# Kernel optimization log

Hardware: AMD Instinct MI355X
Metric: run time of the kernel (lower is better)

## Reference

```python
import jax, jax.numpy as jnp
import numpy as np

# Fixed deterministic sample of 8 offsets from the radius-4 ring (|dx|>1 or |dy|>1, not center).
# The torch module samples these randomly each step; we freeze them for reproducibility.
OFFSETS = [(-4, -4), (-4, -1), (-4, 2), (-3, 4), (-2, -3), (2, 3), (3, -2), (4, 4)]

B, C, H, W = 4, 16, 512, 512
DM, GH = 16, 32  # d_model, gating_hidden


def conv1x1(x, w, b):
    # 1x1 conv == per-pixel matmul: x [B,Cin,H,W], w [Cout,Cin], b [Cout]
    return jnp.einsum('bchw,dc->bdhw', x, w) + b[None, :, None, None]


def setup_inputs() -> dict:
    key = jax.random.key(0)
    ks = jax.random.split(key, 12)
    s_c = 1.0 / np.sqrt(C)
    s_2c = 1.0 / np.sqrt(2 * C)
    s_gh = 1.0 / np.sqrt(GH)
    return {
        'x': jax.random.normal(ks[0], (B, C, H, W), jnp.float32),
        'qw': jax.random.normal(ks[1], (DM, C), jnp.float32) * s_c,
        'qb': jnp.zeros((DM,), jnp.float32),
        'kw': jax.random.normal(ks[2], (DM, C), jnp.float32) * s_c,
        'kb': jnp.zeros((DM,), jnp.float32),
        'mw': jax.random.normal(ks[3], (C, C), jnp.float32) * s_c,
        'mb': jnp.zeros((C,), jnp.float32),
        'scaling': jnp.asarray(np.sqrt(DM), jnp.float32),
        'g1w': jax.random.normal(ks[4], (GH, 2 * C), jnp.float32) * s_2c,
        'g1b': jnp.zeros((GH,), jnp.float32),
        'g2w': jax.random.normal(ks[5], (C, GH), jnp.float32) * s_gh,
        'g2b': jnp.zeros((C,), jnp.float32),
    }


def reference(x, qw, qb, kw, kb, mw, mb, scaling, g1w, g1b, g2w, g2b):
    Q = conv1x1(x, qw, qb)            # [B,DM,H,W]
    K = conv1x1(x, kw, kb)            # [B,DM,H,W]
    M = conv1x1(x, mw, mb)            # [B,C,H,W]
    Q_pooled = Q.mean(axis=(2, 3))    # [B,DM]
    K_pooled = K.mean(axis=(2, 3))    # [B,DM]
    # torch.roll is circular, so the spatial mean of a rolled K equals K_pooled exactly;
    # every offset therefore produces the identical affinity (same math, cheaper).
    attn = (Q_pooled * K_pooled).sum(axis=1) / (scaling + 1e-6)   # [B]
    n = len(OFFSETS)
    # roll-based neighbor gather of messages: [n,B,C,H,W]
    msgs = jnp.stack([jnp.roll(M, (dy, dx), axis=(2, 3)) for dy, dx in OFFSETS], axis=0)
    affinities = jnp.broadcast_to(attn[None, :], (n, attn.shape[0]))  # [n,B]
    w = jax.nn.softmax(affinities, axis=0)[:, :, None, None, None]    # [n,B,1,1,1]
    agg = (msgs * w).sum(axis=0)                                      # [B,C,H,W]
    concat = jnp.concatenate([x, agg], axis=1)                        # [B,2C,H,W]
    hidden = jax.nn.relu(conv1x1(concat, g1w, g1b))                   # [B,GH,H,W]
    gate = jax.nn.sigmoid(conv1x1(hidden, g2w, g2b))                  # [B,C,H,W]
    return agg * gate
```

## Files before the change

kernel.cpp:

```cpp
#include <hip/hip_runtime.h>


#define HW 262144

typedef _Float16 half8  __attribute__((ext_vector_type(8)));
typedef float    f32x4  __attribute__((ext_vector_type(4)));

#define MFMA16(A, B, C) __builtin_amdgcn_mfma_f32_16x16x32_f16((A), (B), (C), 0, 0, 0)

__global__ __launch_bounds__(256, 2) void ga_main(
    const float* __restrict__ x,
    const float* __restrict__ mw,  const float* __restrict__ mb,
    const float* __restrict__ g1w, const float* __restrict__ g1b,
    const float* __restrict__ g2w, const float* __restrict__ g2b,
    float* __restrict__ out)
{
  constexpr int DY[8] = {-4, -4, -4, -3, -2, 2, 3, 4};
  constexpr int DX[8] = {-4, -1,  2,  4, -3, 3, -2, 4};

  __shared__ _Float16 u_s[4 * 64 * 40];
  __shared__ float    w1a[32 * 16];
  __shared__ float    b1s[32];

  const int tid  = threadIdx.x;
  const int wv   = tid >> 6, lane = tid & 63;
  const int q    = lane >> 4, m = lane & 15;

  for (int idx = tid; idx < 512; idx += 256) {
    const int j = idx >> 4, c = idx & 15;
    float s = 0.f;
#pragma unroll
    for (int t2 = 0; t2 < 16; ++t2)
      s += g1w[j * 32 + 16 + t2] * mw[t2 * 16 + c];
    w1a[idx] = s;
  }
  if (tid < 32) {
    float s = g1b[tid];
#pragma unroll
    for (int t2 = 0; t2 < 16; ++t2)
      s += g1w[tid * 32 + 16 + t2] * mb[t2];
    b1s[tid] = s;
  }
  __syncthreads();

  const int j0 = 8 * (m >> 2) + (m & 3);
  const int j1 = j0 + 4;
  half8 aAg_h, aAg_l, aH0_h, aH0_l, aH1_h, aH1_l, aG2_h, aG2_l;
#pragma unroll
  for (int e = 0; e < 8; ++e) {
    const int kk = 8 * q + e;
    float v0 = 0.f;
    if (kk >= 16) v0 = mw[m * 16 + (kk - 16)];
    _Float16 h = (_Float16)v0;
    aAg_h[e] = h; aAg_l[e] = (_Float16)(v0 - (float)h);

    float v1, v2;
    if (kk < 16) { v1 = g1w[j0 * 32 + kk];        v2 = g1w[j1 * 32 + kk]; }
    else         { v1 = w1a[j0 * 16 + (kk - 16)]; v2 = w1a[j1 * 16 + (kk - 16)]; }
    h = (_Float16)v1; aH0_h[e] = h; aH0_l[e] = (_Float16)(v1 - (float)h);
    h = (_Float16)v2; aH1_h[e] = h; aH1_l[e] = (_Float16)(v2 - (float)h);

    const float v3 = g2w[m * 32 + kk];
    h = (_Float16)v3; aG2_h[e] = h; aG2_l[e] = (_Float16)(v3 - (float)h);
  }
  f32x4 bias0, bias1, bias2, bias3;
#pragma unroll
  for (int rg = 0; rg < 4; ++rg) {
    bias0[rg] = mb[4 * q + rg];
    bias1[rg] = b1s[8 * q + rg];
    bias2[rg] = b1s[8 * q + 4 + rg];
    bias3[rg] = g2b[4 * q + rg];
  }

  const int swz = ((blockIdx.x & 7) << 9) | (blockIdx.x >> 3);
  const int b   = swz >> 10;
  const int rem = swz & 1023;
  const int row = rem >> 1;
  const int colbase = ((rem & 1) << 8) + wv * 64;
  const int cw  = colbase + lane;

  const float* xb = x + b * 16 * HW;
  unsigned off[8];
#pragma unroll
  for (int i = 0; i < 8; ++i)
    off[i] = ((row - DY[i]) & 511) * 512 + ((cw - DX[i]) & 511);
  const unsigned ctr = row * 512 + cw;

  float xc[16], xa[16];
#pragma unroll
  for (int c = 0; c < 16; ++c) {
    const float* xp = xb + c * HW;
    xc[c] = xp[ctr];
    float s = 0.f;
#pragma unroll
    for (int i = 0; i < 8; ++i) s += xp[off[i]];
    xa[c] = s * 0.125f;
  }

  _Float16* ub = u_s + (wv * 64 + lane) * 40;
#pragma unroll
  for (int j = 0; j < 4; ++j) {
    half8 v;
#pragma unroll
    for (int e = 0; e < 8; ++e) {
      const int k = j * 8 + e;
      v[e] = (_Float16)((k < 16) ? xc[k] : xa[k - 16]);
    }
    *(half8*)(ub + j * 8) = v;
  }

  const _Float16* ubase = u_s + wv * 64 * 40;
  half8 bf[4];
#pragma unroll
  for (int g = 0; g < 4; ++g)
    bf[g] = *(const half8*)(ubase + (g * 16 + m) * 40 + q * 8);

  float* ob = out + b * 16 * HW + row * 512 + colbase;
  const f32x4 z = {0.f, 0.f, 0.f, 0.f};

#pragma unroll
  for (int g = 0; g < 4; ++g) {
    f32x4 acc_a  = MFMA16(aAg_l, bf[g], z);
    acc_a        = MFMA16(aAg_h, bf[g], acc_a);
    f32x4 acc_h0 = MFMA16(aH0_l, bf[g], z);
    acc_h0       = MFMA16(aH0_h, bf[g], acc_h0);
    f32x4 acc_h1 = MFMA16(aH1_l, bf[g], z);
    acc_h1       = MFMA16(aH1_h, bf[g], acc_h1);

    half8 gB;
#pragma unroll
    for (int rg = 0; rg < 4; ++rg) {
      gB[rg]     = (_Float16)fmaxf(acc_h0[rg] + bias1[rg], 0.f);
      gB[4 + rg] = (_Float16)fmaxf(acc_h1[rg] + bias2[rg], 0.f);
    }

    f32x4 acc_g = MFMA16(aG2_l, gB, z);
    acc_g       = MFMA16(aG2_h, gB, acc_g);

#pragma unroll
    for (int rg = 0; rg < 4; ++rg) {
      const float ag = acc_a[rg] + bias0[rg];
      const float gp = acc_g[rg] + bias3[rg];
      const float gt = __builtin_amdgcn_rcpf(1.f + __expf(-gp));
      ob[(4 * q + rg) * HW + g * 16 + m] = ag * gt;
    }
  }
}

extern "C" void kernel_launch(void* const* d_in, const int* in_sizes, int n_in,
                              void* d_out, int out_size, void* d_ws, size_t ws_size,
                              hipStream_t stream) {
  const float* x   = (const float*)d_in[0];
  const float* mw  = (const float*)d_in[5];
  const float* mb  = (const float*)d_in[6];
  const float* g1w = (const float*)d_in[8];
  const float* g1b = (const float*)d_in[9];
  const float* g2w = (const float*)d_in[10];
  const float* g2b = (const float*)d_in[11];
  float* out = (float*)d_out;

  ga_main<<<4096, 256, 0, stream>>>(x, mw, mb, g1w, g1b, g2w, g2b, out);
}
```

Measured before the change: 188.3 us.

## Process two pixels per lane with float2 gathers and halve block size

Each lane now handles two adjacent columns, loading the center and the eight neighbor samples as float2 vector loads. A wave-uniform fallback to scalar loads covers the case where the column wrap would split a pair. Blocks shrink to two waves, each covering 128 columns with eight MFMA groups, and B fragments are read from LDS inside the loop. The aim is to cut the number of load instructions and raise per-lane work, at the cost of higher register pressure and fewer threads per block.

```diff
diff --git a/kernel.cpp b/kernel.cpp
--- a/kernel.cpp
+++ b/kernel.cpp
@@ -2,13 +2,14 @@
 
 
 #define HW 262144
+#define WD 512
 
-typedef _Float16 half8  __attribute__((ext_vector_type(8)));
-typedef float    f32x4  __attribute__((ext_vector_type(4)));
+typedef _Float16 half8 __attribute__((ext_vector_type(8)));
+typedef float    f32x4 __attribute__((ext_vector_type(4)));
 
 #define MFMA16(A, B, C) __builtin_amdgcn_mfma_f32_16x16x32_f16((A), (B), (C), 0, 0, 0)
 
-__global__ __launch_bounds__(256, 2) void ga_main(
+__global__ __launch_bounds__(128) void ga_main(
     const float* __restrict__ x,
     const float* __restrict__ mw,  const float* __restrict__ mb,
     const float* __restrict__ g1w, const float* __restrict__ g1b,
@@ -18,7 +19,7 @@
   constexpr int DY[8] = {-4, -4, -4, -3, -2, 2, 3, 4};
   constexpr int DX[8] = {-4, -1,  2,  4, -3, 3, -2, 4};
 
-  __shared__ _Float16 u_s[4 * 64 * 40];
+  __shared__ _Float16 u_s[2][128 * 40];
   __shared__ float    w1a[32 * 16];
   __shared__ float    b1s[32];
 
@@ -26,7 +27,7 @@
   const int wv   = tid >> 6, lane = tid & 63;
   const int q    = lane >> 4, m = lane & 15;
 
-  for (int idx = tid; idx < 512; idx += 256) {
+  for (int idx = tid; idx < 512; idx += 128) {
     const int j = idx >> 4, c = idx & 15;
     float s = 0.f;
 #pragma unroll
@@ -76,56 +77,69 @@
   const int b   = swz >> 10;
   const int rem = swz & 1023;
   const int row = rem >> 1;
-  const int colbase = ((rem & 1) << 8) + wv * 64;
-  const int cw  = colbase + lane;
+  const int wavecol = ((rem & 1) << 8) + (wv << 7);
+  const int w0  = wavecol + (lane << 1);
 
   const float* xb = x + b * 16 * HW;
-  unsigned off[8];
+
+  unsigned idxA[8], idxB[8];
+  bool lsplit = false;
 #pragma unroll
-  for (int i = 0; i < 8; ++i)
-    off[i] = ((row - DY[i]) & 511) * 512 + ((cw - DX[i]) & 511);
-  const unsigned ctr = row * 512 + cw;
+  for (int i = 0; i < 8; ++i) {
+    const unsigned ro = ((row - DY[i]) & 511) * WD;
+    const int baseA = (w0 - DX[i]) & 511;
+    idxA[i] = ro + baseA;
+    idxB[i] = ro + ((w0 + 1 - DX[i]) & 511);
+    if (baseA == 511) lsplit = true;
+  }
+  const bool wsplit = __any(lsplit);
+  const unsigned ctr = row * WD + w0;
 
-  float xc[16], xa[16];
+  half8 uc0lo, uc0hi, ua0lo, ua0hi, uc1lo, uc1hi, ua1lo, ua1hi;
 #pragma unroll
   for (int c = 0; c < 16; ++c) {
     const float* xp = xb + c * HW;
-    xc[c] = xp[ctr];
-    float s = 0.f;
+    const float2 cv = *(const float2*)(xp + ctr);
+    float s0 = 0.f, s1 = 0.f;
+    if (!wsplit) {
 #pragma unroll
-    for (int i = 0; i < 8; ++i) s += xp[off[i]];
-    xa[c] = s * 0.125f;
+      for (int i = 0; i < 8; ++i) {
+        const float2 v = *(const float2*)(xp + idxA[i]);
+        s0 += v.x; s1 += v.y;
+      }
+    } else {
+#pragma unroll
+      for (int i = 0; i < 8; ++i) { s0 += xp[idxA[i]]; s1 += xp[idxB[i]]; }
+    }
+    const _Float16 hc0 = (_Float16)cv.x;
+    const _Float16 hc1 = (_Float16)cv.y;
+    const _Float16 ha0 = (_Float16)(s0 * 0.125f);
+    const _Float16 ha1 = (_Float16)(s1 * 0.125f);
+    if (c < 8) { uc0lo[c] = hc0; uc1lo[c] = hc1; ua0lo[c] = ha0; ua1lo[c] = ha1; }
+    else { uc0hi[c - 8] = hc0; uc1hi[c - 8] = hc1; ua0hi[c - 8] = ha0; ua1hi[c - 8] = ha1; }
   }
 
-  _Float16* ub = u_s + (wv * 64 + lane) * 40;
-#pragma unroll
-  for (int j = 0; j < 4; ++j) {
-    half8 v;
-#pragma unroll
-    for (int e = 0; e < 8; ++e) {
-      const int k = j * 8 + e;
-      v[e] = (_Float16)((k < 16) ? xc[k] : xa[k - 16]);
-    }
-    *(half8*)(ub + j * 8) = v;
-  }
+  _Float16* u0 = &u_s[wv][(lane << 1) * 40];
+  _Float16* u1 = u0 + 40;
+  *(half8*)(u0 +  0) = uc0lo;  *(half8*)(u0 +  8) = uc0hi;
+  *(half8*)(u0 + 16) = ua0lo;  *(half8*)(u0 + 24) = ua0hi;
+  *(half8*)(u1 +  0) = uc1lo;  *(half8*)(u1 +  8) = uc1hi;
+  *(half8*)(u1 + 16) = ua1lo;  *(half8*)(u1 + 24) = ua1hi;
 
-  const _Float16* ubase = u_s + wv * 64 * 40;
-  half8 bf[4];
-#pragma unroll
-  for (int g = 0; g < 4; ++g)
-    bf[g] = *(const half8*)(ubase + (g * 16 + m) * 40 + q * 8);
-
-  float* ob = out + b * 16 * HW + row * 512 + colbase;
+  const _Float16* ubase = u_s[wv];
+  float* ob = out + b * 16 * HW + row * WD + wavecol;
   const f32x4 z = {0.f, 0.f, 0.f, 0.f};
 
 #pragma unroll
-  for (int g = 0; g < 4; ++g) {
-    f32x4 acc_a  = MFMA16(aAg_l, bf[g], z);
-    acc_a        = MFMA16(aAg_h, bf[g], acc_a);
-    f32x4 acc_h0 = MFMA16(aH0_l, bf[g], z);
-    acc_h0       = MFMA16(aH0_h, bf[g], acc_h0);
-    f32x4 acc_h1 = MFMA16(aH1_l, bf[g], z);
-    acc_h1       = MFMA16(aH1_h, bf[g], acc_h1);
+  for (int g = 0; g < 8; ++g) {
+    const half8 bf = *(const half8*)(ubase + (g * 16 + m) * 40 + q * 8);
+
+    f32x4 acc_a  = MFMA16(aAg_l, bf, z);
+    acc_a        = MFMA16(aAg_h, bf, acc_a);
+    f32x4 acc_h0 = MFMA16(aH0_l, bf, z);
+    acc_h0       = MFMA16(aH0_h, bf, acc_h0);
+    f32x4 acc_h1 = MFMA16(aH1_l, bf, z);
+    acc_h1       = MFMA16(aH1_h, bf, acc_h1);
 
     half8 gB;
 #pragma unroll
@@ -159,5 +173,5 @@
   const float* g2b = (const float*)d_in[11];
   float* out = (float*)d_out;
 
-  ga_main<<<4096, 256, 0, stream>>>(x, mw, mb, g1w, g1b, g2w, g2b, out);
+  ga_main<<<4096, 128, 0, stream>>>(x, mw, mb, g1w, g1b, g2w, g2b, out);
 }
```

After: 190.2 us. About the same (+1.0%).
